# Optimization experiments

Measured on AMD Instinct MI355X. Metric: run time of the kernel, lower is better.

## Reference

```python
import jax, jax.numpy as jnp
import numpy as np

VOCAB = 32000
H = 256        # d_model
L = 4096       # l_max
N = 64         # SSM state size (S4 default)
CH = 1         # channels
BATCH = 8
PAD = 0        # pad_token_id
DT_MIN, DT_MAX = 0.001, 0.1


def setup_inputs() -> dict:
    key = jax.random.key(0)
    ks = jax.random.split(key, 8)
    input_ids = jax.random.randint(ks[0], (BATCH, L), 0, VOCAB)
    embedding = (jax.random.normal(ks[1], (VOCAB, H), dtype=jnp.float32) * 0.02).at[PAD].set(0.0)
    # S4D-Lin style initialization
    log_dt = jnp.log(DT_MIN) + jax.random.uniform(ks[2], (H,), dtype=jnp.float32) * (np.log(DT_MAX) - np.log(DT_MIN))
    A_log_re = jnp.full((H, N), np.log(0.5), dtype=jnp.float32)          # A_real = -exp(A_log_re)
    A_im = jnp.broadcast_to(np.pi * jnp.arange(N, dtype=jnp.float32), (H, N)).copy()
    B_re = jnp.ones((H, N), dtype=jnp.float32)
    B_im = jnp.zeros((H, N), dtype=jnp.float32)
    # bidirectional => 2*CH output channels for C
    C_re = jax.random.normal(ks[3], (2 * CH, H, N), dtype=jnp.float32) * (0.5 ** 0.5)
    C_im = jax.random.normal(ks[4], (2 * CH, H, N), dtype=jnp.float32) * (0.5 ** 0.5)
    D = jax.random.normal(ks[5], (CH, H), dtype=jnp.float32)
    W_out = jax.random.normal(ks[6], (2 * H, CH * H), dtype=jnp.float32) / np.sqrt(CH * H)
    b_out = jnp.zeros((2 * H,), dtype=jnp.float32)
    return {"input_ids": input_ids, "embedding": embedding, "log_dt": log_dt,
            "A_log_re": A_log_re, "A_im": A_im, "B_re": B_re, "B_im": B_im,
            "C_re": C_re, "C_im": C_im, "D": D, "W_out": W_out, "b_out": b_out}


def _s4_forward(input_ids, embedding, log_dt, A_log_re, A_im, B_re, B_im, C_re, C_im, D, W_out, b_out):
    u = embedding[input_ids]                 # (B, L, H) embedding lookup
    u = jnp.swapaxes(u, 1, 2)                # (B, H, L) transposed=True
    dt = jnp.exp(log_dt)                     # (H,)
    A = -jnp.exp(A_log_re) + 1j * A_im       # (H, N) Hurwitz diagonal SSM
    dtA = dt[:, None] * A                    # (H, N)
    dA = jnp.exp(dtA)                        # discrete A (ZOH)
    dB = (B_re + 1j * B_im) * (dA - 1.0) / A # discrete B (ZOH), (H, N)
    Cc = C_re + 1j * C_im                    # (2*CH, H, N)
    # Vandermonde kernel: K[c,h,l] = 2*Re(sum_n C[c,h,n] dB[h,n] exp(dtA[h,n]*l))
    pos = jnp.arange(L, dtype=jnp.float32)
    vand = jnp.exp(dtA[:, :, None] * pos)    # (H, N, L) complex
    K = 2.0 * jnp.einsum('chn,hn,hnl->chl', Cc, dB, vand).real  # (2*CH, H, L)
    # bidirectional: causal kernel + flipped anti-causal kernel, conv length 2L
    k0, k1 = K[:CH], K[CH:]
    k = jnp.pad(k0, ((0, 0), (0, 0), (0, L))) + jnp.pad(k1[..., ::-1], ((0, 0), (0, 0), (L, 0)))
    k_f = jnp.fft.rfft(k, n=2 * L)           # (CH, H, L+1)
    u_f = jnp.fft.rfft(u, n=2 * L)           # (B, H, L+1)
    y = jnp.fft.irfft(u_f[:, None] * k_f[None], n=2 * L)[..., :L]  # (B, CH, H, L)
    y = y + u[:, None, :, :] * D[None, :, :, None]                 # skip connection
    y = y.reshape(u.shape[0], CH * H, L)
    y = jax.nn.gelu(y, approximate=False)
    z = jnp.einsum('oi,bil->bol', W_out, y) + b_out[None, :, None]  # (B, 2H, L)
    y = z[:, :H] * jax.nn.sigmoid(z[:, H:])                          # GLU
    y = jnp.swapaxes(y, 1, 2)                # (B, L, H)
    return y[:, -1]                           # pool='last' -> (B, H)


def reference(input_ids, embedding, log_dt, A_log_re, A_im, B_re, B_im, C_re, C_im, D, W_out, b_out):
    return _s4_forward(input_ids, embedding, log_dt, A_log_re, A_im, B_re, B_im, C_re, C_im, D, W_out, b_out)
```

## Files before the change

kernel.cpp:

```cpp
#include <hip/hip_runtime.h>
#include <math.h>

#define HH 256
#define NN 64
#define LL 4096
#define BB 8
#define CC 8
#define LC (LL / CC)
#define GG 16
#define HN (HH * NN)

typedef __attribute__((ext_vector_type(2))) float pf2;
typedef __attribute__((ext_vector_type(16))) float f16v;
typedef const __attribute__((address_space(4))) f16v* cf16p;


__global__ __launch_bounds__(256) void frontend_kernel(
    const int* __restrict__ ids, const float* __restrict__ emb,
    const float* __restrict__ log_dt, const float* __restrict__ A_log_re,
    const float* __restrict__ A_im, const float* __restrict__ B_re,
    const float* __restrict__ B_im, const float* __restrict__ C_re,
    const float* __restrict__ C_im,
    float2* __restrict__ dAo, float2* __restrict__ wo, float2* __restrict__ pw,
    float* __restrict__ u_ws) {
    __shared__ int ids_s[64];
    __shared__ float tb[64][257];
    int t = threadIdx.x;
    if (blockIdx.x < BB * 64) {
        int b = blockIdx.x >> 6;
        int tile = blockIdx.x & 63;
        int w4 = t >> 6, lane = t & 63;
        if (t < 64) ids_s[t] = ids[b * LL + tile * 64 + t];
        __syncthreads();
        #pragma unroll 4
        for (int r = w4; r < 64; r += 4) {
            float4 v = ((const float4*)(emb + (long)ids_s[r] * HH))[lane];
            tb[r][lane * 4 + 0] = v.x;
            tb[r][lane * 4 + 1] = v.y;
            tb[r][lane * 4 + 2] = v.z;
            tb[r][lane * 4 + 3] = v.w;
        }
        __syncthreads();
        #pragma unroll 4
        for (int r2 = 0; r2 < 64; ++r2) {
            int h = w4 * 64 + r2;
            u_ws[(b * HH + h) * LL + tile * 64 + lane] = tb[lane][h];
        }
    } else {
        int idx = (blockIdx.x - BB * 64) * 256 + t;
        int h = idx >> 6;
        float dt = expf(log_dt[h]);
        float Are = -expf(A_log_re[idx]);
        float Aim = A_im[idx];
        float ea = expf(dt * Are);
        float sn, cs;
        sincosf(dt * Aim, &sn, &cs);
        float dAre = ea * cs, dAim = ea * sn;
        float numre = dAre - 1.0f, numim = dAim;
        float den = Are * Are + Aim * Aim;
        float qre = (numre * Are + numim * Aim) / den;
        float qim = (numim * Are - numre * Aim) / den;
        float bre = B_re[idx], bim = B_im[idx];
        float dBre = bre * qre - bim * qim;
        float dBim = bre * qim + bim * qre;
        float cre = C_re[idx], cim = C_im[idx];
        dAo[idx] = make_float2(dAre, dAim);
        wo[idx] = make_float2(2.0f * (cre * dBre - cim * dBim),
                              2.0f * (cre * dBim + cim * dBre));
        float pr = dAre, pi = dAim;
        #pragma unroll
        for (int k = 0; k < 9; ++k) {
            float nr = pr * pr - pi * pi;
            float ni = 2.0f * pr * pi;
            pr = nr; pi = ni;
        }
        float qr = 1.0f, qi = 0.0f;
        #pragma unroll
        for (int k = 0; k < CC; ++k) {
            pw[k * HN + idx] = make_float2(qr, qi);
            float nr = qr * pr - qi * pi, ni = qr * pi + qi * pr;
            qr = nr; qi = ni;
        }
    }
}

__global__ __launch_bounds__(512) void scan_kernel(
    const float* __restrict__ u_ws, const float2* __restrict__ dAv,
    const float2* __restrict__ pw, const float2* __restrict__ wv,
    const float* __restrict__ D, float* __restrict__ g) {
    __shared__ float2 part[CC][NN];
    int t = threadIdx.x;
    int c = __builtin_amdgcn_readfirstlane(t >> 6);
    int n = t & 63;
    int bh = blockIdx.x;
    int h = bh & (HH - 1);

    float2 dA = dAv[h * NN + n];
    pf2 Q[GG];
    pf2 q; q.x = 1.0f; q.y = 0.0f;
    #pragma unroll
    for (int k = 0; k < GG; ++k) {
        Q[GG - 1 - k] = q;
        pf2 nq;
        nq.x = q.x * dA.x - q.y * dA.y;
        nq.y = q.x * dA.y + q.y * dA.x;
        q = nq;
    }
    pf2 Rp; Rp.x = q.x; Rp.y = q.x;
    pf2 Rm; Rm.x = -q.y; Rm.y = q.y;

    cf16p src = (cf16p)(unsigned long long)(u_ws + bh * LL + c * LC);
    pf2 P; P.x = 0.0f; P.y = 0.0f;
    #pragma unroll 4
    for (int j = 0; j < LC / GG; ++j) {
        f16v u = src[j];
        pf2 T; T.x = 0.0f; T.y = 0.0f;
        #pragma unroll
        for (int k = 0; k < GG; ++k) {
            pf2 ub; ub.x = u[k]; ub.y = u[k];
            T = __builtin_elementwise_fma(ub, Q[k], T);
        }
        pf2 Ps; Ps.x = P.y; Ps.y = P.x;
        P = __builtin_elementwise_fma(P, Rp, __builtin_elementwise_fma(Ps, Rm, T));
    }
    float2 sc = pw[(CC - 1 - c) * HN + h * NN + n];
    part[c][n] = make_float2(P.x * sc.x - P.y * sc.y,
                             P.x * sc.y + P.y * sc.x);
    __syncthreads();

    if (c == 0) {
        float Sr = 0.0f, Si = 0.0f;
        #pragma unroll
        for (int cc = 0; cc < CC; ++cc) {
            float2 v = part[cc][n];
            Sr += v.x; Si += v.y;
        }
        float2 wc = wv[h * NN + n];
        float contrib = fmaf(wc.x, Sr, -(wc.y * Si));
        #pragma unroll
        for (int m = 32; m > 0; m >>= 1) contrib += __shfl_xor(contrib, m);
        if (n == 0) {
            float y = contrib + u_ws[bh * LL + LL - 1] * D[h];
            float ge = 0.5f * y * (1.0f + erff(y * 0.70710678118654752f));
            g[bh] = ge;
        }
    }
}

__global__ __launch_bounds__(256) void out_kernel(
    const float* __restrict__ g, const float* __restrict__ W,
    const float* __restrict__ bvec, float* __restrict__ out) {
    int b = blockIdx.x >> 7;
    int tile = blockIdx.x & 127;
    int t = threadIdx.x;
    int w = t >> 6, lane = t & 63;
    __shared__ float gs[HH];
    __shared__ float zb[4];
    gs[t] = g[b * HH + t];
    __syncthreads();
    int hh = tile * 2 + (w >> 1);
    int o = (w & 1) * HH + hh;
    float4 wv4 = ((const float4*)(W + o * HH))[lane];
    float4 gv4 = ((const float4*)gs)[lane];
    float p = wv4.x * gv4.x + wv4.y * gv4.y + wv4.z * gv4.z + wv4.w * gv4.w;
    #pragma unroll
    for (int m = 32; m > 0; m >>= 1) p += __shfl_xor(p, m);
    if (lane == 0) zb[w] = p + bvec[o];
    __syncthreads();
    if (t < 2) {
        int hq = tile * 2 + t;
        float z1 = zb[t * 2 + 0];
        float z2 = zb[t * 2 + 1];
        out[b * HH + hq] = z1 * (1.0f / (1.0f + expf(-z2)));
    }
}

extern "C" void kernel_launch(void* const* d_in, const int* in_sizes, int n_in,
                              void* d_out, int out_size, void* d_ws, size_t ws_size,
                              hipStream_t stream) {
    const int* input_ids = (const int*)d_in[0];
    const float* embedding = (const float*)d_in[1];
    const float* log_dt = (const float*)d_in[2];
    const float* A_log_re = (const float*)d_in[3];
    const float* A_im = (const float*)d_in[4];
    const float* B_re = (const float*)d_in[5];
    const float* B_im = (const float*)d_in[6];
    const float* C_re = (const float*)d_in[7];
    const float* C_im = (const float*)d_in[8];
    const float* D = (const float*)d_in[9];
    const float* W_out = (const float*)d_in[10];
    const float* b_out = (const float*)d_in[11];
    float* out = (float*)d_out;

    float* ws = (float*)d_ws;
    float2* dAv = (float2*)ws;
    float2* wv = (float2*)(ws + 32768);
    float2* pw = (float2*)(ws + 65536);
    float* u_ws = ws + 327680;
    float* g = ws + 10813440;

    frontend_kernel<<<BB * 64 + HN / 256, 256, 0, stream>>>(
        input_ids, embedding, log_dt, A_log_re, A_im, B_re, B_im, C_re, C_im,
        dAv, wv, pw, u_ws);

    scan_kernel<<<BB * HH, 512, 0, stream>>>(u_ws, dAv, pw, wv, D, g);

    out_kernel<<<BB * 128, 256, 0, stream>>>(g, W_out, b_out, out);
}
```

Measured before the change: 133.6 us.

## Double-buffer embedding transpose in 64-column chunks with 512-thread blocks

The embedding gather-transpose now processes the 256-wide hidden dimension in four 64-column chunks through a double-buffered shared tile. The global load of the next chunk overlaps the transposed write-out of the current one, and the stores become float4 vectorized instead of scalar. Blocks grow to 512 threads and shared memory use shrinks, which aims at better latency hiding and occupancy. The cost is an extra barrier per chunk and more complex indexing.

```diff
diff --git a/kernel.cpp b/kernel.cpp
--- a/kernel.cpp
+++ b/kernel.cpp
@@ -15,7 +15,7 @@
 typedef const __attribute__((address_space(4))) f16v* cf16p;
 
 
-__global__ __launch_bounds__(256) void frontend_kernel(
+__global__ __launch_bounds__(512) void frontend_kernel(
     const int* __restrict__ ids, const float* __restrict__ emb,
     const float* __restrict__ log_dt, const float* __restrict__ A_log_re,
     const float* __restrict__ A_im, const float* __restrict__ B_re,
@@ -23,31 +23,70 @@
     const float* __restrict__ C_im,
     float2* __restrict__ dAo, float2* __restrict__ wo, float2* __restrict__ pw,
     float* __restrict__ u_ws) {
-    __shared__ int ids_s[64];
-    __shared__ float tb[64][257];
     int t = threadIdx.x;
     if (blockIdx.x < BB * 64) {
+        __shared__ int ids_s[64];
+        __shared__ float tb[2][64][65];
         int b = blockIdx.x >> 6;
         int tile = blockIdx.x & 63;
-        int w4 = t >> 6, lane = t & 63;
+        int w = t >> 6;
+        int lane = t & 63;
+        int rq = lane >> 4;
+        int k = lane & 15;
         if (t < 64) ids_s[t] = ids[b * LL + tile * 64 + t];
         __syncthreads();
-        #pragma unroll 4
-        for (int r = w4; r < 64; r += 4) {
-            float4 v = ((const float4*)(emb + (long)ids_s[r] * HH))[lane];
-            tb[r][lane * 4 + 0] = v.x;
-            tb[r][lane * 4 + 1] = v.y;
-            tb[r][lane * 4 + 2] = v.z;
-            tb[r][lane * 4 + 3] = v.w;
+        {
+            int r0 = w * 8 + rq;
+            float4 v0 = *(const float4*)(emb + (long)ids_s[r0] * HH + 4 * k);
+            float4 v1 = *(const float4*)(emb + (long)ids_s[r0 + 4] * HH + 4 * k);
+            tb[0][r0][4 * k + 0] = v0.x;
+            tb[0][r0][4 * k + 1] = v0.y;
+            tb[0][r0][4 * k + 2] = v0.z;
+            tb[0][r0][4 * k + 3] = v0.w;
+            tb[0][r0 + 4][4 * k + 0] = v1.x;
+            tb[0][r0 + 4][4 * k + 1] = v1.y;
+            tb[0][r0 + 4][4 * k + 2] = v1.z;
+            tb[0][r0 + 4][4 * k + 3] = v1.w;
         }
         __syncthreads();
-        #pragma unroll 4
-        for (int r2 = 0; r2 < 64; ++r2) {
-            int h = w4 * 64 + r2;
-            u_ws[(b * HH + h) * LL + tile * 64 + lane] = tb[lane][h];
+        #pragma unroll
+        for (int c4 = 0; c4 < 4; ++c4) {
+            int cur = c4 & 1;
+            float4 v0, v1;
+            if (c4 < 3) {
+                int r0 = w * 8 + rq;
+                v0 = *(const float4*)(emb + (long)ids_s[r0] * HH +
+                                      (c4 + 1) * 64 + 4 * k);
+                v1 = *(const float4*)(emb + (long)ids_s[r0 + 4] * HH +
+                                      (c4 + 1) * 64 + 4 * k);
+            }
+            #pragma unroll
+            for (int it = 0; it < 2; ++it) {
+                int hq = w * 8 + it * 4 + rq;
+                int s0 = 4 * k;
+                float4 o;
+                o.x = tb[cur][s0 + 0][hq];
+                o.y = tb[cur][s0 + 1][hq];
+                o.z = tb[cur][s0 + 2][hq];
+                o.w = tb[cur][s0 + 3][hq];
+                *(float4*)(u_ws + ((long)(b * HH + c4 * 64 + hq)) * LL +
+                           tile * 64 + s0) = o;
+            }
+            if (c4 < 3) {
+                int r0 = w * 8 + rq;
+                tb[cur ^ 1][r0][4 * k + 0] = v0.x;
+                tb[cur ^ 1][r0][4 * k + 1] = v0.y;
+                tb[cur ^ 1][r0][4 * k + 2] = v0.z;
+                tb[cur ^ 1][r0][4 * k + 3] = v0.w;
+                tb[cur ^ 1][r0 + 4][4 * k + 0] = v1.x;
+                tb[cur ^ 1][r0 + 4][4 * k + 1] = v1.y;
+                tb[cur ^ 1][r0 + 4][4 * k + 2] = v1.z;
+                tb[cur ^ 1][r0 + 4][4 * k + 3] = v1.w;
+            }
+            __syncthreads();
         }
     } else {
-        int idx = (blockIdx.x - BB * 64) * 256 + t;
+        int idx = (blockIdx.x - BB * 64) * 512 + t;
         int h = idx >> 6;
         float dt = expf(log_dt[h]);
         float Are = -expf(A_log_re[idx]);
@@ -69,15 +108,15 @@
                               2.0f * (cre * dBim + cim * dBre));
         float pr = dAre, pi = dAim;
         #pragma unroll
-        for (int k = 0; k < 9; ++k) {
+        for (int kk = 0; kk < 9; ++kk) {
             float nr = pr * pr - pi * pi;
             float ni = 2.0f * pr * pi;
             pr = nr; pi = ni;
         }
         float qr = 1.0f, qi = 0.0f;
         #pragma unroll
-        for (int k = 0; k < CC; ++k) {
-            pw[k * HN + idx] = make_float2(qr, qi);
+        for (int kk = 0; kk < CC; ++kk) {
+            pw[kk * HN + idx] = make_float2(qr, qi);
             float nr = qr * pr - qi * pi, ni = qr * pi + qi * pr;
             qr = nr; qi = ni;
         }
@@ -199,7 +238,7 @@
     float* u_ws = ws + 327680;
     float* g = ws + 10813440;
 
-    frontend_kernel<<<BB * 64 + HN / 256, 256, 0, stream>>>(
+    frontend_kernel<<<BB * 64 + HN / 512, 512, 0, stream>>>(
         input_ids, embedding, log_dt, A_log_re, A_im, B_re, B_im, C_re, C_im,
         dAv, wv, pw, u_ws);
 
```

Measured after the change: 134.4 us. About the same (+0.6%).
